# Optimization experiments

Measured on AMD Instinct MI355X. Metric: run time of the kernel, lower is better.

## Reference

```python
import jax, jax.numpy as jnp
import numpy as np

BATCH, S, D = 96, 1024, 64  # B*H batched attention-score BMM (GPT-2: H=12, d_head=64)
ALPHA = 0.0008138020833333334  # a_scale * b_scale
A_ZP = 12.0
B_ZP = -7.0


def setup_inputs() -> dict:
    key = jax.random.key(0)
    k1, k2 = jax.random.split(key)
    # int8 quantized activations (stored as int8, matching torch int8 buffers)
    x = jax.random.randint(k1, (BATCH, S, D), -128, 128, dtype=jnp.int32).astype(jnp.int8)
    y = jax.random.randint(k2, (BATCH, D, S), -128, 128, dtype=jnp.int32).astype(jnp.int8)
    return {
        "x": x,
        "y": y,
        "a_zp": jnp.float32(A_ZP),
        "b_zp": jnp.float32(B_ZP),
        "alpha": jnp.float32(ALPHA),
    }


def reference(x, y, a_zp, b_zp, alpha):
    # (x - a_zp) @ (y - b_zp) * alpha, computed in fp32 exactly as the torch module:
    # int8 -> int32 -> float, subtract zero points, batched matmul, scale.
    a = x.astype(jnp.float32) - a_zp  # [BATCH, S, D]
    b = y.astype(jnp.float32) - b_zp  # [BATCH, D, S]
    return jnp.einsum('bsd,bdt->bst', a, b) * alpha  # [BATCH, S, S] fp32
```

## Files before the change

### kernel.cpp

```cpp
#include <hip/hip_runtime.h>
#include <stdint.h>

typedef __attribute__((ext_vector_type(4))) int int4v;
typedef __attribute__((ext_vector_type(4))) float float4v;

#define NB 96
#define SS 1024
#define DD 64
#define TILE_U32 2048
#define NBT (NB * 8)

__device__ __forceinline__ int PSI(int r) { return ((r & 3) << 2) | (r >> 2); }

static __device__ __forceinline__ uint32_t pack4(uint32_t a, uint32_t b,
                                                 uint32_t c, uint32_t d) {
    uint32_t lo = __builtin_amdgcn_perm(b, a, 0x00000400u);
    uint32_t hi = __builtin_amdgcn_perm(d, c, 0x00000400u);
    return __builtin_amdgcn_perm(hi, lo, 0x05040100u);
}

__global__ __launch_bounds__(256) void pack_kernel(
    const int* __restrict__ Y, uint32_t* __restrict__ Yp)
{
    __shared__ uint32_t sb[TILE_U32];
    const int tid = threadIdx.x;
    const int t2 = blockIdx.x;
    const int b = t2 >> 3, nt = t2 & 7;
    const int* Yb = Y + (size_t)b * (DD * SS) + nt * 128;
    const int tw = tid & 31;
    const int r  = tw & 15, wn = tw >> 4;
    const int4v* srcBase = (const int4v*)Yb + tw;
    #pragma unroll
    for (int it = 0; it < 2; ++it) {
        const int kw = (tid >> 5) + 8 * it;
        const int4v* src = srcBase + (size_t)(4 * kw) * (SS / 4);
        int4v r0 = src[0];
        int4v r1 = src[SS / 4];
        int4v r2 = src[2 * (SS / 4)];
        int4v r3 = src[3 * (SS / 4)];
        const int slot = kw ^ PSI(r);
        #pragma unroll
        for (int n = 0; n < 4; ++n) {
            uint32_t pk = pack4((uint32_t)r0[n], (uint32_t)r1[n],
                                (uint32_t)r2[n], (uint32_t)r3[n]);
            sb[(wn * 64 + n * 16 + r) * 16 + slot] = pk;
        }
    }
    __syncthreads();
    uint32_t* dst = Yp + (size_t)t2 * TILE_U32;
    ((int4v*)dst)[tid]       = ((const int4v*)sb)[tid];
    ((int4v*)dst)[tid + 256] = ((const int4v*)sb)[tid + 256];
}

__global__ __launch_bounds__(256) void bmm_i8zp_kernel(
    const int* __restrict__ X,
    const uint32_t* __restrict__ Yp,
    const float* __restrict__ azp,
    const float* __restrict__ bzp,
    const float* __restrict__ alp,
    float* __restrict__ out)
{
    __shared__ uint32_t sb[TILE_U32];

    const int tid = threadIdx.x;
    const int bid = (blockIdx.x & 7) * 768 + (blockIdx.x >> 3);
    const int b   = bid >> 6;
    const int mt  = (bid >> 3) & 7;
    const int nt  = bid & 7;
    const int rowbase = mt * 128;
    const int colbase = nt * 128;

    const float az = *azp, bz = *bzp, al = *alp;
    const float czk = az * bz * (float)DD;

    {
        const int4v* Yimg = (const int4v*)(Yp + ((size_t)b * 8 + nt) * TILE_U32);
        ((int4v*)sb)[tid]       = Yimg[tid];
        ((int4v*)sb)[tid + 256] = Yimg[tid + 256];
    }

    const int wid  = tid >> 6;
    const int lane = tid & 63;
    const int wm = wid >> 1, wn = wid & 1;
    const int rr = lane & 15, qq = lane >> 4;

    int4v aF[4];
    {
        #pragma unroll
        for (int m = 0; m < 4; ++m) {
            const int4v* arow = (const int4v*)(X +
                (size_t)(b * SS + rowbase + wm * 64 + m * 16 + rr) * DD + qq * 16);
            int4v w0 = arow[0], w1 = arow[1], w2 = arow[2], w3 = arow[3];
            int4v v;
            v[0] = (int)pack4((uint32_t)w0[0], (uint32_t)w0[1], (uint32_t)w0[2], (uint32_t)w0[3]);
            v[1] = (int)pack4((uint32_t)w1[0], (uint32_t)w1[1], (uint32_t)w1[2], (uint32_t)w1[3]);
            v[2] = (int)pack4((uint32_t)w2[0], (uint32_t)w2[1], (uint32_t)w2[2], (uint32_t)w2[3]);
            v[3] = (int)pack4((uint32_t)w3[0], (uint32_t)w3[1], (uint32_t)w3[2], (uint32_t)w3[3]);
            aF[m] = v;
        }
    }
    __syncthreads();

    int4v bF[4];
    #pragma unroll
    for (int n = 0; n < 4; ++n) {
        const int u = wn * 64 + n * 16 + rr;
        int4v v;
        #pragma unroll
        for (int c = 0; c < 4; ++c)
            v[c] = (int)sb[u * 16 + ((qq * 4 + c) ^ PSI(rr))];
        bF[n] = v;
    }

    const int4v ones = {0x01010101, 0x01010101, 0x01010101, 0x01010101};
    const int4v zero = {0, 0, 0, 0};

    float cyI[4];
    #pragma unroll
    for (int n = 0; n < 4; ++n) {
        int4v cy = __builtin_amdgcn_mfma_i32_16x16x64_i8(ones, bF[n], zero, 0, 0, 0);
        cyI[n] = az * (float)cy[0];
    }

    float* outb = out + (size_t)b * SS * SS;
    const int cb = colbase + wn * 64 + 4 * rr;

    #pragma unroll
    for (int m = 0; m < 4; ++m) {
        int4v rx = __builtin_amdgcn_mfma_i32_16x16x64_i8(aF[m], ones, zero, 0, 0, 0);
        int4v acc[4];
        #pragma unroll
        for (int n = 0; n < 4; ++n)
            acc[n] = __builtin_amdgcn_mfma_i32_16x16x64_i8(aF[m], bF[n], zero, 0, 0, 0);

        const int rb = rowbase + wm * 64 + m * 16 + qq * 4;
        #pragma unroll
        for (int j = 0; j < 4; ++j) {
            const float corr = czk - bz * (float)rx[j];
            float4v v;
            #pragma unroll
            for (int n = 0; n < 4; ++n)
                v[n] = ((float)acc[n][j] - cyI[n] + corr) * al;
            __builtin_nontemporal_store(
                v, (float4v*)(outb + (size_t)(rb + j) * SS + cb));
        }
    }
}

extern "C" void kernel_launch(void* const* d_in, const int* in_sizes, int n_in,
                              void* d_out, int out_size, void* d_ws, size_t ws_size,
                              hipStream_t stream)
{
    const int* X = (const int*)d_in[0];
    const int* Y = (const int*)d_in[1];
    const float* azp = (const float*)d_in[2];
    const float* bzp = (const float*)d_in[3];
    const float* alp = (const float*)d_in[4];
    float* out = (float*)d_out;

    uint32_t* Yp = (uint32_t*)d_ws;

    hipLaunchKernelGGL(pack_kernel, dim3(NBT), dim3(256), 0, stream, Y, Yp);
    hipLaunchKernelGGL(bmm_i8zp_kernel, dim3(NB * 8 * 8), dim3(256), 0, stream,
                       X, Yp, azp, bzp, alp, out);
}
```

Measured before the change: 77.12 us.

## Fuse Y packing into BMM kernel and loop blocks over row tiles

Removes the separate pack kernel and workspace round-trip by packing each Y column tile into LDS inside the matmul kernel. Each block now owns one (batch, column-tile) pair and iterates over all 8 row tiles, loading and packing X fragments per step, so the Y packing is done once per block. This removes a launch and the extra global traffic for packed Y. In exchange the grid shrinks eightfold, which reduces parallelism and latency hiding for the store-bound epilogue.

```diff
diff --git a/kernel.cpp b/kernel.cpp
--- a/kernel.cpp
+++ b/kernel.cpp
@@ -8,7 +8,6 @@
 #define SS 1024
 #define DD 64
 #define TILE_U32 2048
-#define NBT (NB * 8)
 
 __device__ __forceinline__ int PSI(int r) { return ((r & 3) << 2) | (r >> 2); }
 
@@ -19,42 +18,9 @@
     return __builtin_amdgcn_perm(hi, lo, 0x05040100u);
 }
 
-__global__ __launch_bounds__(256) void pack_kernel(
-    const int* __restrict__ Y, uint32_t* __restrict__ Yp)
-{
-    __shared__ uint32_t sb[TILE_U32];
-    const int tid = threadIdx.x;
-    const int t2 = blockIdx.x;
-    const int b = t2 >> 3, nt = t2 & 7;
-    const int* Yb = Y + (size_t)b * (DD * SS) + nt * 128;
-    const int tw = tid & 31;
-    const int r  = tw & 15, wn = tw >> 4;
-    const int4v* srcBase = (const int4v*)Yb + tw;
-    #pragma unroll
-    for (int it = 0; it < 2; ++it) {
-        const int kw = (tid >> 5) + 8 * it;
-        const int4v* src = srcBase + (size_t)(4 * kw) * (SS / 4);
-        int4v r0 = src[0];
-        int4v r1 = src[SS / 4];
-        int4v r2 = src[2 * (SS / 4)];
-        int4v r3 = src[3 * (SS / 4)];
-        const int slot = kw ^ PSI(r);
-        #pragma unroll
-        for (int n = 0; n < 4; ++n) {
-            uint32_t pk = pack4((uint32_t)r0[n], (uint32_t)r1[n],
-                                (uint32_t)r2[n], (uint32_t)r3[n]);
-            sb[(wn * 64 + n * 16 + r) * 16 + slot] = pk;
-        }
-    }
-    __syncthreads();
-    uint32_t* dst = Yp + (size_t)t2 * TILE_U32;
-    ((int4v*)dst)[tid]       = ((const int4v*)sb)[tid];
-    ((int4v*)dst)[tid + 256] = ((const int4v*)sb)[tid + 256];
-}
-
 __global__ __launch_bounds__(256) void bmm_i8zp_kernel(
     const int* __restrict__ X,
-    const uint32_t* __restrict__ Yp,
+    const int* __restrict__ Y,
     const float* __restrict__ azp,
     const float* __restrict__ bzp,
     const float* __restrict__ alp,
@@ -63,43 +29,42 @@
     __shared__ uint32_t sb[TILE_U32];
 
     const int tid = threadIdx.x;
-    const int bid = (blockIdx.x & 7) * 768 + (blockIdx.x >> 3);
-    const int b   = bid >> 6;
-    const int mt  = (bid >> 3) & 7;
+    const int bid = (blockIdx.x & 7) * 96 + (blockIdx.x >> 3);
+    const int b   = bid >> 3;
     const int nt  = bid & 7;
-    const int rowbase = mt * 128;
     const int colbase = nt * 128;
 
     const float az = *azp, bz = *bzp, al = *alp;
     const float czk = az * bz * (float)DD;
 
     {
-        const int4v* Yimg = (const int4v*)(Yp + ((size_t)b * 8 + nt) * TILE_U32);
-        ((int4v*)sb)[tid]       = Yimg[tid];
-        ((int4v*)sb)[tid + 256] = Yimg[tid + 256];
+        const int* Yb = Y + (size_t)b * (DD * SS) + colbase;
+        const int tw = tid & 31;
+        const int r  = tw & 15, wnp = tw >> 4;
+        const int4v* srcBase = (const int4v*)Yb + tw;
+        #pragma unroll
+        for (int it = 0; it < 2; ++it) {
+            const int kw = (tid >> 5) + 8 * it;
+            const int4v* src = srcBase + (size_t)(4 * kw) * (SS / 4);
+            int4v r0 = src[0];
+            int4v r1 = src[SS / 4];
+            int4v r2 = src[2 * (SS / 4)];
+            int4v r3 = src[3 * (SS / 4)];
+            const int slot = kw ^ PSI(r);
+            #pragma unroll
+            for (int n = 0; n < 4; ++n) {
+                uint32_t pk = pack4((uint32_t)r0[n], (uint32_t)r1[n],
+                                    (uint32_t)r2[n], (uint32_t)r3[n]);
+                sb[(wnp * 64 + n * 16 + r) * 16 + slot] = pk;
+            }
+        }
     }
+    __syncthreads();
 
     const int wid  = tid >> 6;
     const int lane = tid & 63;
     const int wm = wid >> 1, wn = wid & 1;
     const int rr = lane & 15, qq = lane >> 4;
-
-    int4v aF[4];
-    {
-        #pragma unroll
-        for (int m = 0; m < 4; ++m) {
-            const int4v* arow = (const int4v*)(X +
-                (size_t)(b * SS + rowbase + wm * 64 + m * 16 + rr) * DD + qq * 16);
-            int4v w0 = arow[0], w1 = arow[1], w2 = arow[2], w3 = arow[3];
-            int4v v;
-            v[0] = (int)pack4((uint32_t)w0[0], (uint32_t)w0[1], (uint32_t)w0[2], (uint32_t)w0[3]);
-            v[1] = (int)pack4((uint32_t)w1[0], (uint32_t)w1[1], (uint32_t)w1[2], (uint32_t)w1[3]);
-            v[2] = (int)pack4((uint32_t)w2[0], (uint32_t)w2[1], (uint32_t)w2[2], (uint32_t)w2[3]);
-            v[3] = (int)pack4((uint32_t)w3[0], (uint32_t)w3[1], (uint32_t)w3[2], (uint32_t)w3[3]);
-            aF[m] = v;
-        }
-    }
-    __syncthreads();
 
     int4v bF[4];
     #pragma unroll
@@ -124,25 +89,37 @@
 
     float* outb = out + (size_t)b * SS * SS;
     const int cb = colbase + wn * 64 + 4 * rr;
+    const int* Xw = X + ((size_t)b * SS + wm * 64 + rr) * DD + qq * 16;
 
-    #pragma unroll
-    for (int m = 0; m < 4; ++m) {
-        int4v rx = __builtin_amdgcn_mfma_i32_16x16x64_i8(aF[m], ones, zero, 0, 0, 0);
-        int4v acc[4];
+    for (int mt = 0; mt < 8; ++mt) {
+        const int rowbase = mt * 128;
         #pragma unroll
-        for (int n = 0; n < 4; ++n)
-            acc[n] = __builtin_amdgcn_mfma_i32_16x16x64_i8(aF[m], bF[n], zero, 0, 0, 0);
+        for (int m = 0; m < 4; ++m) {
+            const int4v* arow = (const int4v*)(Xw + (size_t)(rowbase + m * 16) * DD);
+            int4v w0 = arow[0], w1 = arow[1], w2 = arow[2], w3 = arow[3];
+            int4v aF;
+            aF[0] = (int)pack4((uint32_t)w0[0], (uint32_t)w0[1], (uint32_t)w0[2], (uint32_t)w0[3]);
+            aF[1] = (int)pack4((uint32_t)w1[0], (uint32_t)w1[1], (uint32_t)w1[2], (uint32_t)w1[3]);
+            aF[2] = (int)pack4((uint32_t)w2[0], (uint32_t)w2[1], (uint32_t)w2[2], (uint32_t)w2[3]);
+            aF[3] = (int)pack4((uint32_t)w3[0], (uint32_t)w3[1], (uint32_t)w3[2], (uint32_t)w3[3]);
 
-        const int rb = rowbase + wm * 64 + m * 16 + qq * 4;
-        #pragma unroll
-        for (int j = 0; j < 4; ++j) {
-            const float corr = czk - bz * (float)rx[j];
-            float4v v;
+            int4v rx = __builtin_amdgcn_mfma_i32_16x16x64_i8(aF, ones, zero, 0, 0, 0);
+            int4v acc[4];
             #pragma unroll
             for (int n = 0; n < 4; ++n)
-                v[n] = ((float)acc[n][j] - cyI[n] + corr) * al;
-            __builtin_nontemporal_store(
-                v, (float4v*)(outb + (size_t)(rb + j) * SS + cb));
+                acc[n] = __builtin_amdgcn_mfma_i32_16x16x64_i8(aF, bF[n], zero, 0, 0, 0);
+
+            const int rb = rowbase + wm * 64 + m * 16 + qq * 4;
+            #pragma unroll
+            for (int j = 0; j < 4; ++j) {
+                const float corr = czk - bz * (float)rx[j];
+                float4v v;
+                #pragma unroll
+                for (int n = 0; n < 4; ++n)
+                    v[n] = ((float)acc[n][j] - cyI[n] + corr) * al;
+                __builtin_nontemporal_store(
+                    v, (float4v*)(outb + (size_t)(rb + j) * SS + cb));
+            }
         }
     }
 }
@@ -158,9 +135,6 @@
     const float* alp = (const float*)d_in[4];
     float* out = (float*)d_out;
 
-    uint32_t* Yp = (uint32_t*)d_ws;
-
-    hipLaunchKernelGGL(pack_kernel, dim3(NBT), dim3(256), 0, stream, Y, Yp);
-    hipLaunchKernelGGL(bmm_i8zp_kernel, dim3(NB * 8 * 8), dim3(256), 0, stream,
-                       X, Yp, azp, bzp, alp, out);
+    hipLaunchKernelGGL(bmm_i8zp_kernel, dim3(NB * 8), dim3(256), 0, stream,
+                       X, Y, azp, bzp, alp, out);
 }
```

Measured after the change: 85.87 us. 11.3% more time.
